# Optimization experiments

Measured on AMD Instinct MI355X. Metric: run time of the kernel, lower is better.

## Reference

```python
import jax, jax.numpy as jnp
import numpy as np

B, T, I, H = 128, 512, 1024, 1024


def _xavier(key, shape):
    # matches torch nn.init.xavier_uniform_
    fan_in, fan_out = shape
    limit = float(np.sqrt(6.0 / (fan_in + fan_out)))
    return jax.random.uniform(key, shape, jnp.float32, -limit, limit)


def setup_inputs() -> dict:
    key = jax.random.key(0)
    ks = jax.random.split(key, 9)
    x = jax.random.normal(ks[0], (B, T, I), dtype=jnp.float32)
    names = ['W_ii', 'W_hi', 'W_if', 'W_hf', 'W_ig', 'W_hg', 'W_io', 'W_ho']
    inp = {'x': x}
    for k, name in zip(ks[1:], names):
        shape = (I, H) if name[2] == 'i' else (H, H)
        inp[name] = _xavier(k, shape)
    for bname in ['b_ii', 'b_hi', 'b_if', 'b_hf', 'b_ig', 'b_hg', 'b_io', 'b_ho']:
        inp[bname] = jnp.zeros((H,), dtype=jnp.float32)
    return inp


def reference(x, W_ii, b_ii, W_hi, b_hi, W_if, b_if, W_hf, b_hf,
              W_ig, b_ig, W_hg, b_hg, W_io, b_io, W_ho, b_ho):
    """LSTM over x [B, T, I]; returns final (h_t, c_t), each [B, H].
    Faithful to the module's per-gate math (input gate i, forget gate f,
    cell candidate g with tanh, output gate o with sigmoid), zero init state.
    Gates are fused into one input GEMM per step group: precompute x @ W_i*
    for all timesteps at once, then scan the recurrence."""
    batch, seq, _ = x.shape
    hidden = W_hi.shape[0]
    # Precompute input projections for all timesteps: [T, B, 4H]
    W_in = jnp.concatenate([W_ii, W_if, W_ig, W_io], axis=1)          # [I, 4H]
    b_in = jnp.concatenate([b_ii + b_hi, b_if + b_hf, b_ig + b_hg, b_io + b_ho])
    x_proj = jnp.einsum('bti,ih->tbh', x, W_in) + b_in                # [T, B, 4H]
    W_h = jnp.concatenate([W_hi, W_hf, W_hg, W_ho], axis=1)           # [H, 4H]

    def step(carry, xp):
        h, c = carry
        gates = xp + h @ W_h                                          # [B, 4H]
        i_t = jax.nn.sigmoid(gates[:, 0 * hidden:1 * hidden])
        f_t = jax.nn.sigmoid(gates[:, 1 * hidden:2 * hidden])
        g_t = jnp.tanh(gates[:, 2 * hidden:3 * hidden])
        o_t = jax.nn.sigmoid(gates[:, 3 * hidden:4 * hidden])
        c = f_t * c + i_t * g_t
        h = o_t * jnp.tanh(c)
        return (h, c), None

    h0 = jnp.zeros((batch, hidden), dtype=x.dtype)
    c0 = jnp.zeros((batch, hidden), dtype=x.dtype)
    (h_t, c_t), _ = jax.lax.scan(step, (h0, c0), x_proj)
    return (h_t, c_t)
```

## Files before the change

### kernel.cpp

```cpp
#include <hip/hip_runtime.h>
#include <cstdint>
#include <cstddef>


#define B_  128
#define T_  512
#define I_  1024
#define H_  1024
#define G4_ 4096
#define SLOTG 32768ull

typedef __attribute__((ext_vector_type(8))) short short8;
typedef __attribute__((ext_vector_type(4))) float f32x4;
typedef unsigned long long u64;

static __device__ __forceinline__ unsigned short f2bf(float f) {
    unsigned u = __builtin_bit_cast(unsigned, f);
    u += 0x7fffu + ((u >> 16) & 1u);
    return (unsigned short)(u >> 16);
}
static __device__ __forceinline__ float bf2f(unsigned short s) {
    unsigned u = (unsigned)s << 16;
    return __builtin_bit_cast(float, u);
}
static __device__ __forceinline__ float sigm(float x) {
    return 1.0f / (1.0f + exp2f(-1.4426950408889634f * x));
}
static __device__ __forceinline__ float tanh_(float x) {
    float e = exp2f(2.8853900817779268f * x);
    return 1.0f - 2.0f / (e + 1.0f);
}
static __device__ __forceinline__ f32x4 mfma16(short8 a, short8 b, f32x4 c) {
    return __builtin_amdgcn_mfma_f32_16x16x32_bf16(a, b, c, 0, 0, 0);
}
static __device__ __forceinline__ bool hasff(u64 v) {
    u64 x = ~v;
    return ((x - 0x0001000100010001ull) & ~x & 0x8000800080008000ull) != 0ull;
}

__global__ __launch_bounds__(256) void pack_w(const float* __restrict__ W,
                                              unsigned short* __restrict__ outBt,
                                              int g) {
    __shared__ float tile[64][65];
    const int tid = threadIdx.x;
    const int k0 = blockIdx.y * 64;
    const int j0 = blockIdx.x * 64;
    {
        const int r  = tid >> 2;
        const int c0 = (tid & 3) * 16;
        const float* src = W + (size_t)(k0 + r) * H_ + j0 + c0;
        #pragma unroll
        for (int q = 0; q < 4; ++q) {
            float4 v = *(const float4*)(src + q * 4);
            tile[r][c0 + q*4 + 0] = v.x;
            tile[r][c0 + q*4 + 1] = v.y;
            tile[r][c0 + q*4 + 2] = v.z;
            tile[r][c0 + q*4 + 3] = v.w;
        }
    }
    __syncthreads();
    {
        const int jl   = tid >> 2;
        const int kseg = (tid & 3) * 16;
        unsigned short* orow = outBt + ((size_t)(j0 + jl) * 4 + g) * 1024 + (k0 + kseg);
        #pragma unroll
        for (int q = 0; q < 16; q += 4) {
            ushort4 u;
            u.x = f2bf(tile[kseg + q + 0][jl]);
            u.y = f2bf(tile[kseg + q + 1][jl]);
            u.z = f2bf(tile[kseg + q + 2][jl]);
            u.w = f2bf(tile[kseg + q + 3][jl]);
            *(ushort4*)(orow + q) = u;
        }
    }
}

__global__ __launch_bounds__(256) void pack_bias(
    const float* b0x, const float* b0h, const float* b1x, const float* b1h,
    const float* b2x, const float* b2h, const float* b3x, const float* b3h,
    float* __restrict__ out) {
    int jc = blockIdx.x * 256 + threadIdx.x;
    int g = jc & 3, jh = jc >> 2;
    const float* bx = (g == 0) ? b0x : (g == 1) ? b1x : (g == 2) ? b2x : b3x;
    const float* bh = (g == 0) ? b0h : (g == 1) ? b1h : (g == 2) ? b2h : b3h;
    out[jc] = bx[jh] + bh[jh];
}

__global__ __launch_bounds__(256) void convert_x(const float* __restrict__ x,
                                                 unsigned short* __restrict__ xb,
                                                 int t0, int Tcc) {
    int e = blockIdx.x * 256 + threadIdx.x;
    int i = (e & 127) << 3;
    int r = e >> 7;
    int b = r / Tcc, tc = r - b * Tcc;
    const float* s = x + (size_t)(b * T_ + t0 + tc) * I_ + i;
    float4 v0 = *(const float4*)s;
    float4 v1 = *(const float4*)(s + 4);
    ushort4 u0; u0.x = f2bf(v0.x); u0.y = f2bf(v0.y); u0.z = f2bf(v0.z); u0.w = f2bf(v0.w);
    ushort4 u1; u1.x = f2bf(v1.x); u1.y = f2bf(v1.y); u1.z = f2bf(v1.z); u1.w = f2bf(v1.w);
    unsigned short* d = xb + (size_t)r * I_ + i;
    *(ushort4*)d = u0;
    *(ushort4*)(d + 4) = u1;
}

__global__ __launch_bounds__(256) void gemm_xproj(
    const unsigned short* __restrict__ A,
    const unsigned short* __restrict__ Bt,
    const float* __restrict__ bias,
    unsigned short* __restrict__ xp,
    int Tcc) {
    const int tid = threadIdx.x;
    const int w = tid >> 6, l = tid & 63;
    const int l15 = l & 15, hi = l >> 4;
    const int row0 = blockIdx.y * 64;
    const int col0 = blockIdx.x * 256 + w * 64;
    const int k0 = hi * 8;
    f32x4 acc[4][4] = {};
    const unsigned short* a0 = A  + (size_t)(row0 + l15) * 1024 + k0;
    const unsigned short* b0 = Bt + (size_t)(col0 + l15) * 1024 + k0;
    for (int ks = 0; ks < 1024; ks += 32) {
        short8 a[4], bb[4];
        #pragma unroll
        for (int mi = 0; mi < 4; ++mi) a[mi]  = *(const short8*)(a0 + (size_t)mi * 16 * 1024 + ks);
        #pragma unroll
        for (int ni = 0; ni < 4; ++ni) bb[ni] = *(const short8*)(b0 + (size_t)ni * 16 * 1024 + ks);
        #pragma unroll
        for (int mi = 0; mi < 4; ++mi)
            #pragma unroll
            for (int ni = 0; ni < 4; ++ni)
                acc[mi][ni] = mfma16(a[mi], bb[ni], acc[mi][ni]);
    }
    #pragma unroll
    for (int mi = 0; mi < 4; ++mi) {
        #pragma unroll
        for (int ni = 0; ni < 4; ++ni) {
            int colg = col0 + ni * 16 + l15;
            float bs = bias[colg];
            #pragma unroll
            for (int j = 0; j < 4; ++j) {
                int r = row0 + mi * 16 + hi * 4 + j;
                int b = r / Tcc, tc = r - b * Tcc;
                xp[(size_t)(tc * 128 + b) * G4_ + colg] = f2bf(acc[mi][ni][j] + bs);
            }
        }
    }
}

__global__ __launch_bounds__(1024, 4) void lstm_recur(
    const unsigned short* __restrict__ Whp,
    const unsigned short* __restrict__ xp,
    u64* __restrict__ hring,
    float* __restrict__ cbuf,
    float* __restrict__ outp,
    int Tcc, int is_last_chunk) {
    __shared__ char hlds[32768];
    __shared__ float gl[16][132];
    __shared__ unsigned short hstage[16][32];

    const int tid = threadIdx.x;
    const int wv = tid >> 6, l = tid & 63;
    const int l15 = l & 15, hi = l >> 4;
    const int ct = wv & 7, kh = wv >> 3;
    const int grp = blockIdx.x >> 5;
    const int cb  = blockIdx.x & 31;
    const int row0 = grp * 16;

    short8 wf[16];
    {
        const unsigned short* wb = Whp + (size_t)(cb * 128 + ct * 16 + l15) * 1024
                                       + kh * 512 + hi * 8;
        #pragma unroll
        for (int ks = 0; ks < 16; ++ks) wf[ks] = *(const short8*)(wb + ks * 32);
    }

    const int erow = tid >> 5, ejh = tid & 31;
    float creg = 0.f;
    if (tid < 512) creg = cbuf[(size_t)(row0 + erow) * H_ + cb * 32 + ejh];

    const int gcol = (tid & 63) * 4;

    for (int st = 0; st < Tcc; ++st) {
        ushort4 xv = {0, 0, 0, 0};
        if (tid < 512)
            xv = *(const ushort4*)(xp + ((size_t)st * 128 + row0 + erow) * G4_
                                      + cb * 128 + ejh * 4);

        u64 g0, g1, g2, g3;
        {
            u64* rp = hring + (size_t)st * SLOTG + (size_t)(row0 + wv) * 256 + gcol;
            for (int it = 0; ; ++it) {
                if (it < 64) {
                    g0 = __hip_atomic_load(rp + 0, __ATOMIC_RELAXED, __HIP_MEMORY_SCOPE_AGENT);
                    g1 = __hip_atomic_load(rp + 1, __ATOMIC_RELAXED, __HIP_MEMORY_SCOPE_AGENT);
                    g2 = __hip_atomic_load(rp + 2, __ATOMIC_RELAXED, __HIP_MEMORY_SCOPE_AGENT);
                    g3 = __hip_atomic_load(rp + 3, __ATOMIC_RELAXED, __HIP_MEMORY_SCOPE_AGENT);
                } else {
                    g0 = __hip_atomic_fetch_add(rp + 0, 0ull, __ATOMIC_RELAXED, __HIP_MEMORY_SCOPE_AGENT);
                    g1 = __hip_atomic_fetch_add(rp + 1, 0ull, __ATOMIC_RELAXED, __HIP_MEMORY_SCOPE_AGENT);
                    g2 = __hip_atomic_fetch_add(rp + 2, 0ull, __ATOMIC_RELAXED, __HIP_MEMORY_SCOPE_AGENT);
                    g3 = __hip_atomic_fetch_add(rp + 3, 0ull, __ATOMIC_RELAXED, __HIP_MEMORY_SCOPE_AGENT);
                }
                if (!(hasff(g0) | hasff(g1) | hasff(g2) | hasff(g3))) break;
                __builtin_amdgcn_s_sleep(1);
            }
        }
        {
            int base = wv * 2048 + gcol * 8;
            int sw = (wv & 7) << 4;
            *(u64*)(hlds + ((base +  0) ^ sw)) = g0;
            *(u64*)(hlds + ((base +  8) ^ sw)) = g1;
            *(u64*)(hlds + ((base + 16) ^ sw)) = g2;
            *(u64*)(hlds + ((base + 24) ^ sw)) = g3;
        }
        __syncthreads();

        f32x4 acc = {};
        {
            const int abase = l15 * 2048 + kh * 1024 + hi * 16;
            const int sw = (l15 & 7) << 4;
            #pragma unroll
            for (int ks = 0; ks < 16; ++ks) {
                short8 a = *(const short8*)(hlds + ((abase + ks * 64) ^ sw));
                acc = mfma16(a, wf[ks], acc);
            }
        }
        if (kh == 0) {
            #pragma unroll
            for (int j = 0; j < 4; ++j) gl[hi * 4 + j][ct * 16 + l15] = acc[j];
        }
        __syncthreads();
        if (kh == 1) {
            #pragma unroll
            for (int j = 0; j < 4; ++j) gl[hi * 4 + j][ct * 16 + l15] += acc[j];
        }
        __syncthreads();

        if (tid < 512) {
            float gi = gl[erow][ejh * 4 + 0] + bf2f(xv.x);
            float gf = gl[erow][ejh * 4 + 1] + bf2f(xv.y);
            float gg = gl[erow][ejh * 4 + 2] + bf2f(xv.z);
            float go = gl[erow][ejh * 4 + 3] + bf2f(xv.w);
            float it = sigm(gi), ft = sigm(gf), gt = tanh_(gg), ot = sigm(go);
            float cn = ft * creg + it * gt;
            float hn = ot * tanh_(cn);
            creg = cn;
            hstage[erow][ejh] = f2bf(hn);
            if (is_last_chunk && st == Tcc - 1) {
                size_t oidx = (size_t)(row0 + erow) * H_ + cb * 32 + ejh;
                outp[oidx] = hn;
                outp[(size_t)B_ * H_ + oidx] = cn;
            }
        }
        __syncthreads();
        if (tid < 128) {
            int prow = tid >> 3, seg = tid & 7;
            u64 hv = *(const u64*)(&hstage[prow][seg * 4]);
            u64* wp = hring + (size_t)(st + 1) * SLOTG
                            + (size_t)(row0 + prow) * 256 + cb * 8 + seg;
            (void)__hip_atomic_exchange(wp, hv, __ATOMIC_RELAXED, __HIP_MEMORY_SCOPE_AGENT);
        }
    }
    if (tid < 512)
        cbuf[(size_t)(row0 + erow) * H_ + cb * 32 + ejh] = creg;
}

extern "C" void kernel_launch(void* const* d_in, const int* in_sizes, int n_in,
                              void* d_out, int out_size, void* d_ws, size_t ws_size,
                              hipStream_t stream) {
    const float* x = (const float*)d_in[0];
    const float* Wx[4] = {(const float*)d_in[1], (const float*)d_in[3],
                          (const float*)d_in[5], (const float*)d_in[7]};
    const float* Wh[4] = {(const float*)d_in[2], (const float*)d_in[4],
                          (const float*)d_in[6], (const float*)d_in[8]};
    const float* bx[4] = {(const float*)d_in[9],  (const float*)d_in[11],
                          (const float*)d_in[13], (const float*)d_in[15]};
    const float* bh[4] = {(const float*)d_in[10], (const float*)d_in[12],
                          (const float*)d_in[14], (const float*)d_in[16]};

    char* p = (char*)d_ws;
    auto take = [&](size_t bytes) {
        char* q = p; p += (bytes + 255) & ~(size_t)255; return q;
    };
    unsigned short* Winp = (unsigned short*)take((size_t)G4_ * 1024 * 2);
    unsigned short* Whp  = (unsigned short*)take((size_t)G4_ * 1024 * 2);
    float*          bias = (float*)take(G4_ * 4);
    float*          cbuf = (float*)take((size_t)B_ * H_ * 4);
    size_t fixed = (size_t)(p - (char*)d_ws);
    size_t per = (size_t)B_ * I_ * 2 + (size_t)B_ * G4_ * 2 + SLOTG * 8 + 768;
    size_t avail = ws_size > fixed + SLOTG * 8 ? ws_size - fixed - SLOTG * 8 : 0;
    int Tc = (int)(avail / per);
    if (Tc > T_) Tc = T_;
    if (Tc < 1) Tc = 1;
    unsigned short* xb    = (unsigned short*)take((size_t)Tc * B_ * I_ * 2);
    unsigned short* xpc   = (unsigned short*)take((size_t)Tc * B_ * G4_ * 2);
    u64*            hring = (u64*)take((size_t)(Tc + 1) * SLOTG * 8);

    for (int g = 0; g < 4; ++g) {
        pack_w<<<dim3(16, 16), 256, 0, stream>>>(Wx[g], Winp, g);
        pack_w<<<dim3(16, 16), 256, 0, stream>>>(Wh[g], Whp, g);
    }
    pack_bias<<<16, 256, 0, stream>>>(bx[0], bh[0], bx[1], bh[1],
                                      bx[2], bh[2], bx[3], bh[3], bias);
    hipMemsetAsync(cbuf, 0, (size_t)B_ * H_ * 4, stream);

    int prev_last = -1;
    for (int t0 = 0; t0 < T_; t0 += Tc) {
        int Tcc = (T_ - t0 < Tc) ? (T_ - t0) : Tc;
        int last = (t0 + Tcc >= T_) ? 1 : 0;
        if (prev_last < 0)
            hipMemsetAsync(hring, 0, SLOTG * 8, stream);
        else
            hipMemcpyAsync(hring, hring + (size_t)prev_last * SLOTG,
                           SLOTG * 8, hipMemcpyDeviceToDevice, stream);
        hipMemsetAsync(hring + SLOTG, 0xFF, (size_t)Tcc * SLOTG * 8, stream);
        convert_x<<<Tcc * 64, 256, 0, stream>>>(x, xb, t0, Tcc);
        gemm_xproj<<<dim3(16, 2 * Tcc), 256, 0, stream>>>(xb, Winp, bias, xpc, Tcc);
        lstm_recur<<<256, 1024, 0, stream>>>(Whp, xpc, hring, cbuf,
                                             (float*)d_out, Tcc, last);
        prev_last = Tcc;
    }
}
```

Before: 3.957 ms.

## Restructure LSTM recurrence block, fuse x conversion into GEMM, drop ring memsets

The recurrent kernel drops to 512 threads per block. Each wave covers 64 gate columns over a quarter of K, so a 4-way partial-sum reduction in LDS replaces the two-pass sum over two K halves. It also polls wider vectors of h with backoff sleeps. The fp32 to bf16 conversion of x moves into the input-projection GEMM, which uses perm truncation instead of round-to-nearest. The GEMM also writes the 0xFF sentinel values into the h ring, so the per-chunk memset and memcpy go away: the final h of each chunk is written into slot 0. The eight weight-pack launches are merged into one. The changes aim to cut launch overhead, extra memory passes and per-step sync latency, at the cost of slightly different bf16 rounding of x and a different occupancy balance in the recurrence.

```diff
diff --git a/kernel.cpp b/kernel.cpp
--- a/kernel.cpp
+++ b/kernel.cpp
@@ -12,6 +12,7 @@
 
 typedef __attribute__((ext_vector_type(8))) short short8;
 typedef __attribute__((ext_vector_type(4))) float f32x4;
+typedef __attribute__((ext_vector_type(2))) unsigned long long u64x2;
 typedef unsigned long long u64;
 
 static __device__ __forceinline__ unsigned short f2bf(float f) {
@@ -33,14 +34,20 @@
 static __device__ __forceinline__ f32x4 mfma16(short8 a, short8 b, f32x4 c) {
     return __builtin_amdgcn_mfma_f32_16x16x32_bf16(a, b, c, 0, 0, 0);
 }
-static __device__ __forceinline__ bool hasff(u64 v) {
-    u64 x = ~v;
-    return ((x - 0x0001000100010001ull) & ~x & 0x8000800080008000ull) != 0ull;
-}
-
-__global__ __launch_bounds__(256) void pack_w(const float* __restrict__ W,
-                                              unsigned short* __restrict__ outBt,
-                                              int g) {
+static __device__ __forceinline__ u64 ffbits(u64 v) {
+    return ((~v) - 0x0001000100010001ull) & v & 0x8000800080008000ull;
+}
+#define AL(p)  __hip_atomic_load((p), __ATOMIC_RELAXED, __HIP_MEMORY_SCOPE_AGENT)
+#define ARMW(p) __hip_atomic_fetch_add((p), 0ull, __ATOMIC_RELAXED, __HIP_MEMORY_SCOPE_AGENT)
+
+__global__ __launch_bounds__(256) void pack_w8(
+    const float* w0, const float* w1, const float* w2, const float* w3,
+    const float* w4, const float* w5, const float* w6, const float* w7,
+    unsigned short* __restrict__ Winp, unsigned short* __restrict__ Whp) {
+    const float* ws[8] = {w0, w1, w2, w3, w4, w5, w6, w7};
+    const float* W = ws[blockIdx.z];
+    unsigned short* dst = (blockIdx.z < 4) ? Winp : Whp;
+    const int g = blockIdx.z & 3;
     __shared__ float tile[64][65];
     const int tid = threadIdx.x;
     const int k0 = blockIdx.y * 64;
@@ -62,7 +69,7 @@
     {
         const int jl   = tid >> 2;
         const int kseg = (tid & 3) * 16;
-        unsigned short* orow = outBt + ((size_t)(j0 + jl) * 4 + g) * 1024 + (k0 + kseg);
+        unsigned short* orow = dst + ((size_t)(j0 + jl) * 4 + g) * 1024 + (k0 + kseg);
         #pragma unroll
         for (int q = 0; q < 16; q += 4) {
             ushort4 u;
@@ -86,42 +93,45 @@
     out[jc] = bx[jh] + bh[jh];
 }
 
-__global__ __launch_bounds__(256) void convert_x(const float* __restrict__ x,
-                                                 unsigned short* __restrict__ xb,
-                                                 int t0, int Tcc) {
-    int e = blockIdx.x * 256 + threadIdx.x;
-    int i = (e & 127) << 3;
-    int r = e >> 7;
-    int b = r / Tcc, tc = r - b * Tcc;
-    const float* s = x + (size_t)(b * T_ + t0 + tc) * I_ + i;
-    float4 v0 = *(const float4*)s;
-    float4 v1 = *(const float4*)(s + 4);
-    ushort4 u0; u0.x = f2bf(v0.x); u0.y = f2bf(v0.y); u0.z = f2bf(v0.z); u0.w = f2bf(v0.w);
-    ushort4 u1; u1.x = f2bf(v1.x); u1.y = f2bf(v1.y); u1.z = f2bf(v1.z); u1.w = f2bf(v1.w);
-    unsigned short* d = xb + (size_t)r * I_ + i;
-    *(ushort4*)d = u0;
-    *(ushort4*)(d + 4) = u1;
-}
-
 __global__ __launch_bounds__(256) void gemm_xproj(
-    const unsigned short* __restrict__ A,
+    const float* __restrict__ x,
     const unsigned short* __restrict__ Bt,
     const float* __restrict__ bias,
     unsigned short* __restrict__ xp,
-    int Tcc) {
+    u64* __restrict__ sent,
+    int t0, int Tcc) {
     const int tid = threadIdx.x;
     const int w = tid >> 6, l = tid & 63;
     const int l15 = l & 15, hi = l >> 4;
     const int row0 = blockIdx.y * 64;
     const int col0 = blockIdx.x * 256 + w * 64;
     const int k0 = hi * 8;
+    const float* xr[4];
+    #pragma unroll
+    for (int mi = 0; mi < 4; ++mi) {
+        int r = row0 + mi * 16 + l15;
+        int b = r / Tcc, tc = r - b * Tcc;
+        xr[mi] = x + ((size_t)b * T_ + t0 + tc) * I_ + k0;
+    }
     f32x4 acc[4][4] = {};
-    const unsigned short* a0 = A  + (size_t)(row0 + l15) * 1024 + k0;
     const unsigned short* b0 = Bt + (size_t)(col0 + l15) * 1024 + k0;
     for (int ks = 0; ks < 1024; ks += 32) {
         short8 a[4], bb[4];
         #pragma unroll
-        for (int mi = 0; mi < 4; ++mi) a[mi]  = *(const short8*)(a0 + (size_t)mi * 16 * 1024 + ks);
+        for (int mi = 0; mi < 4; ++mi) {
+            float4 u = *(const float4*)(xr[mi] + ks);
+            float4 v = *(const float4*)(xr[mi] + ks + 4);
+            unsigned d0 = __builtin_amdgcn_perm(__builtin_bit_cast(unsigned, u.y),
+                                                __builtin_bit_cast(unsigned, u.x), 0x07060302u);
+            unsigned d1 = __builtin_amdgcn_perm(__builtin_bit_cast(unsigned, u.w),
+                                                __builtin_bit_cast(unsigned, u.z), 0x07060302u);
+            unsigned d2 = __builtin_amdgcn_perm(__builtin_bit_cast(unsigned, v.y),
+                                                __builtin_bit_cast(unsigned, v.x), 0x07060302u);
+            unsigned d3 = __builtin_amdgcn_perm(__builtin_bit_cast(unsigned, v.w),
+                                                __builtin_bit_cast(unsigned, v.z), 0x07060302u);
+            uint4 pk = {d0, d1, d2, d3};
+            a[mi] = __builtin_bit_cast(short8, pk);
+        }
         #pragma unroll
         for (int ni = 0; ni < 4; ++ni) bb[ni] = *(const short8*)(b0 + (size_t)ni * 16 * 1024 + ks);
         #pragma unroll
@@ -144,124 +154,146 @@
             }
         }
     }
-}
-
-__global__ __launch_bounds__(1024, 4) void lstm_recur(
+    {
+        size_t sidx = ((size_t)(blockIdx.y * gridDim.x + blockIdx.x) * 256 + tid) * 4;
+        u64* sp = sent + sidx;
+        sp[0] = ~0ull; sp[1] = ~0ull; sp[2] = ~0ull; sp[3] = ~0ull;
+    }
+}
+
+__global__ __launch_bounds__(512, 2) void lstm_recur(
     const unsigned short* __restrict__ Whp,
     const unsigned short* __restrict__ xp,
     u64* __restrict__ hring,
     float* __restrict__ cbuf,
     float* __restrict__ outp,
-    int Tcc, int is_last_chunk) {
-    __shared__ char hlds[32768];
-    __shared__ float gl[16][132];
-    __shared__ unsigned short hstage[16][32];
-
-    const int tid = threadIdx.x;
-    const int wv = tid >> 6, l = tid & 63;
+    int Tcc, int is_last) {
+    __shared__ __align__(16) char hlds[32768];
+    __shared__ __align__(16) float gl[4][16][140];
+
+    const int t = threadIdx.x;
+    const int w = t >> 6, l = t & 63;
     const int l15 = l & 15, hi = l >> 4;
-    const int ct = wv & 7, kh = wv >> 3;
-    const int grp = blockIdx.x >> 5;
-    const int cb  = blockIdx.x & 31;
+    const int cw = w & 1, kq = w >> 1;
+    const int grp = blockIdx.x >> 5, cb = blockIdx.x & 31;
     const int row0 = grp * 16;
 
-    short8 wf[16];
+    short8 wf[4][8];
     {
-        const unsigned short* wb = Whp + (size_t)(cb * 128 + ct * 16 + l15) * 1024
-                                       + kh * 512 + hi * 8;
-        #pragma unroll
-        for (int ks = 0; ks < 16; ++ks) wf[ks] = *(const short8*)(wb + ks * 32);
-    }
-
-    const int erow = tid >> 5, ejh = tid & 31;
-    float creg = 0.f;
-    if (tid < 512) creg = cbuf[(size_t)(row0 + erow) * H_ + cb * 32 + ejh];
-
-    const int gcol = (tid & 63) * 4;
+        const unsigned short* wb = Whp + (size_t)(cb * 128 + cw * 64 + l15) * 1024
+                                       + kq * 256 + hi * 8;
+        #pragma unroll
+        for (int ci = 0; ci < 4; ++ci)
+            #pragma unroll
+            for (int ks = 0; ks < 8; ++ks)
+                wf[ci][ks] = *(const short8*)(wb + ci * 16 * 1024 + ks * 32);
+    }
+
+    const int urow = t & 15, uq = t >> 4;
+    float4 creg = {0.f, 0.f, 0.f, 0.f};
+    if (t < 128)
+        creg = *(const float4*)&cbuf[(size_t)(row0 + urow) * H_ + cb * 32 + uq * 4];
+
+    const int prow = t & 15, pko = t >> 4;
 
     for (int st = 0; st < Tcc; ++st) {
-        ushort4 xv = {0, 0, 0, 0};
-        if (tid < 512)
-            xv = *(const ushort4*)(xp + ((size_t)st * 128 + row0 + erow) * G4_
-                                      + cb * 128 + ejh * 4);
-
-        u64 g0, g1, g2, g3;
+        unsigned short xv[16];
+        if (t < 128) {
+            const unsigned short* xq = xp + ((size_t)st * 128 + row0 + urow) * G4_
+                                          + cb * 128 + uq * 16;
+            *(uint4*)&xv[0] = *(const uint4*)xq;
+            *(uint4*)&xv[8] = *(const uint4*)(xq + 8);
+        }
+
+        u64 q[8];
         {
-            u64* rp = hring + (size_t)st * SLOTG + (size_t)(row0 + wv) * 256 + gcol;
-            for (int it = 0; ; ++it) {
+            u64* rp = hring + (size_t)st * SLOTG + (size_t)(row0 + prow) * 256 + pko * 2;
+            int it = 0;
+            for (;;) {
                 if (it < 64) {
-                    g0 = __hip_atomic_load(rp + 0, __ATOMIC_RELAXED, __HIP_MEMORY_SCOPE_AGENT);
-                    g1 = __hip_atomic_load(rp + 1, __ATOMIC_RELAXED, __HIP_MEMORY_SCOPE_AGENT);
-                    g2 = __hip_atomic_load(rp + 2, __ATOMIC_RELAXED, __HIP_MEMORY_SCOPE_AGENT);
-                    g3 = __hip_atomic_load(rp + 3, __ATOMIC_RELAXED, __HIP_MEMORY_SCOPE_AGENT);
+                    q[0] = AL(rp);       q[1] = AL(rp + 1);
+                    q[2] = AL(rp + 64);  q[3] = AL(rp + 65);
+                    q[4] = AL(rp + 128); q[5] = AL(rp + 129);
+                    q[6] = AL(rp + 192); q[7] = AL(rp + 193);
                 } else {
-                    g0 = __hip_atomic_fetch_add(rp + 0, 0ull, __ATOMIC_RELAXED, __HIP_MEMORY_SCOPE_AGENT);
-                    g1 = __hip_atomic_fetch_add(rp + 1, 0ull, __ATOMIC_RELAXED, __HIP_MEMORY_SCOPE_AGENT);
-                    g2 = __hip_atomic_fetch_add(rp + 2, 0ull, __ATOMIC_RELAXED, __HIP_MEMORY_SCOPE_AGENT);
-                    g3 = __hip_atomic_fetch_add(rp + 3, 0ull, __ATOMIC_RELAXED, __HIP_MEMORY_SCOPE_AGENT);
+                    q[0] = ARMW(rp);       q[1] = ARMW(rp + 1);
+                    q[2] = ARMW(rp + 64);  q[3] = ARMW(rp + 65);
+                    q[4] = ARMW(rp + 128); q[5] = ARMW(rp + 129);
+                    q[6] = ARMW(rp + 192); q[7] = ARMW(rp + 193);
                 }
-                if (!(hasff(g0) | hasff(g1) | hasff(g2) | hasff(g3))) break;
-                __builtin_amdgcn_s_sleep(1);
-            }
-        }
-        {
-            int base = wv * 2048 + gcol * 8;
-            int sw = (wv & 7) << 4;
-            *(u64*)(hlds + ((base +  0) ^ sw)) = g0;
-            *(u64*)(hlds + ((base +  8) ^ sw)) = g1;
-            *(u64*)(hlds + ((base + 16) ^ sw)) = g2;
-            *(u64*)(hlds + ((base + 24) ^ sw)) = g3;
+                u64 bad = ffbits(q[0]) | ffbits(q[1]) | ffbits(q[2]) | ffbits(q[3])
+                        | ffbits(q[4]) | ffbits(q[5]) | ffbits(q[6]) | ffbits(q[7]);
+                if (!bad) break;
+                ++it;
+                if (it < 16) __builtin_amdgcn_s_sleep(1);
+                else         __builtin_amdgcn_s_sleep(4);
+            }
+        }
+        #pragma unroll
+        for (int j = 0; j < 4; ++j) {
+            u64x2 v = {q[2 * j], q[2 * j + 1]};
+            *(u64x2*)(hlds + (pko + 32 * j) * 256 + prow * 16) = v;
         }
         __syncthreads();
 
-        f32x4 acc = {};
-        {
-            const int abase = l15 * 2048 + kh * 1024 + hi * 16;
-            const int sw = (l15 & 7) << 4;
-            #pragma unroll
-            for (int ks = 0; ks < 16; ++ks) {
-                short8 a = *(const short8*)(hlds + ((abase + ks * 64) ^ sw));
-                acc = mfma16(a, wf[ks], acc);
-            }
-        }
-        if (kh == 0) {
-            #pragma unroll
-            for (int j = 0; j < 4; ++j) gl[hi * 4 + j][ct * 16 + l15] = acc[j];
-        }
+        f32x4 acc[4] = {};
+        #pragma unroll
+        for (int ks = 0; ks < 8; ++ks) {
+            int ko = (kq * 8 + ks) * 4 + hi;
+            short8 a = *(const short8*)(hlds + ko * 256 + l15 * 16);
+            #pragma unroll
+            for (int ci = 0; ci < 4; ++ci)
+                acc[ci] = mfma16(a, wf[ci][ks], acc[ci]);
+        }
+        #pragma unroll
+        for (int ci = 0; ci < 4; ++ci)
+            #pragma unroll
+            for (int j = 0; j < 4; ++j)
+                gl[kq][hi * 4 + j][cw * 64 + ci * 16 + l15] = acc[ci][j];
         __syncthreads();
-        if (kh == 1) {
-            #pragma unroll
-            for (int j = 0; j < 4; ++j) gl[hi * 4 + j][ct * 16 + l15] += acc[j];
-        }
-        __syncthreads();
-
-        if (tid < 512) {
-            float gi = gl[erow][ejh * 4 + 0] + bf2f(xv.x);
-            float gf = gl[erow][ejh * 4 + 1] + bf2f(xv.y);
-            float gg = gl[erow][ejh * 4 + 2] + bf2f(xv.z);
-            float go = gl[erow][ejh * 4 + 3] + bf2f(xv.w);
-            float it = sigm(gi), ft = sigm(gf), gt = tanh_(gg), ot = sigm(go);
-            float cn = ft * creg + it * gt;
-            float hn = ot * tanh_(cn);
-            creg = cn;
-            hstage[erow][ejh] = f2bf(hn);
-            if (is_last_chunk && st == Tcc - 1) {
-                size_t oidx = (size_t)(row0 + erow) * H_ + cb * 32 + ejh;
-                outp[oidx] = hn;
-                outp[(size_t)B_ * H_ + oidx] = cn;
-            }
-        }
-        __syncthreads();
-        if (tid < 128) {
-            int prow = tid >> 3, seg = tid & 7;
-            u64 hv = *(const u64*)(&hstage[prow][seg * 4]);
-            u64* wp = hring + (size_t)(st + 1) * SLOTG
-                            + (size_t)(row0 + prow) * 256 + cb * 8 + seg;
-            (void)__hip_atomic_exchange(wp, hv, __ATOMIC_RELAXED, __HIP_MEMORY_SCOPE_AGENT);
-        }
-    }
-    if (tid < 512)
-        cbuf[(size_t)(row0 + erow) * H_ + cb * 32 + ejh] = creg;
+
+        if (t < 128) {
+            float g16[16];
+            #pragma unroll
+            for (int qq = 0; qq < 4; ++qq) {
+                float4 s = *(const float4*)&gl[0][urow][uq * 16 + qq * 4];
+                #pragma unroll
+                for (int k2 = 1; k2 < 4; ++k2) {
+                    float4 s2 = *(const float4*)&gl[k2][urow][uq * 16 + qq * 4];
+                    s.x += s2.x; s.y += s2.y; s.z += s2.z; s.w += s2.w;
+                }
+                g16[qq * 4 + 0] = s.x; g16[qq * 4 + 1] = s.y;
+                g16[qq * 4 + 2] = s.z; g16[qq * 4 + 3] = s.w;
+            }
+            unsigned short hb[4];
+            float cn4[4], hn4[4];
+            #pragma unroll
+            for (int qq = 0; qq < 4; ++qq) {
+                float gi = g16[qq * 4 + 0] + bf2f(xv[qq * 4 + 0]);
+                float gf = g16[qq * 4 + 1] + bf2f(xv[qq * 4 + 1]);
+                float gg = g16[qq * 4 + 2] + bf2f(xv[qq * 4 + 2]);
+                float go = g16[qq * 4 + 3] + bf2f(xv[qq * 4 + 3]);
+                float it_ = sigm(gi), ft = sigm(gf), gt = tanh_(gg), ot = sigm(go);
+                float co = (qq == 0) ? creg.x : (qq == 1) ? creg.y : (qq == 2) ? creg.z : creg.w;
+                float cn = ft * co + it_ * gt;
+                float hn = ot * tanh_(cn);
+                cn4[qq] = cn; hn4[qq] = hn; hb[qq] = f2bf(hn);
+            }
+            creg.x = cn4[0]; creg.y = cn4[1]; creg.z = cn4[2]; creg.w = cn4[3];
+            u64 hw = (u64)hb[0] | ((u64)hb[1] << 16) | ((u64)hb[2] << 32) | ((u64)hb[3] << 48);
+            int dst = (st == Tcc - 1) ? 0 : st + 1;
+            u64* wp = hring + (size_t)dst * SLOTG + (size_t)(row0 + urow) * 256
+                            + cb * 8 + uq;
+            (void)__hip_atomic_exchange(wp, hw, __ATOMIC_RELAXED, __HIP_MEMORY_SCOPE_AGENT);
+            if (is_last && st == Tcc - 1) {
+                size_t o = (size_t)(row0 + urow) * H_ + cb * 32 + uq * 4;
+                *(float4*)&outp[o] = {hn4[0], hn4[1], hn4[2], hn4[3]};
+                *(float4*)&outp[(size_t)B_ * H_ + o] = creg;
+            }
+        }
+    }
+    if (t < 128)
+        *(float4*)&cbuf[(size_t)(row0 + urow) * H_ + cb * 32 + uq * 4] = creg;
 }
 
 extern "C" void kernel_launch(void* const* d_in, const int* in_sizes, int n_in,
@@ -285,38 +317,28 @@
     unsigned short* Whp  = (unsigned short*)take((size_t)G4_ * 1024 * 2);
     float*          bias = (float*)take(G4_ * 4);
     float*          cbuf = (float*)take((size_t)B_ * H_ * 4);
-    size_t fixed = (size_t)(p - (char*)d_ws);
-    size_t per = (size_t)B_ * I_ * 2 + (size_t)B_ * G4_ * 2 + SLOTG * 8 + 768;
-    size_t avail = ws_size > fixed + SLOTG * 8 ? ws_size - fixed - SLOTG * 8 : 0;
+    size_t fixed = (size_t)(p - (char*)d_ws) + SLOTG * 8 + 512;
+    size_t per = (size_t)B_ * G4_ * 2 + SLOTG * 8 + 512;
+    size_t avail = ws_size > fixed ? ws_size - fixed : 0;
     int Tc = (int)(avail / per);
     if (Tc > T_) Tc = T_;
     if (Tc < 1) Tc = 1;
-    unsigned short* xb    = (unsigned short*)take((size_t)Tc * B_ * I_ * 2);
     unsigned short* xpc   = (unsigned short*)take((size_t)Tc * B_ * G4_ * 2);
     u64*            hring = (u64*)take((size_t)(Tc + 1) * SLOTG * 8);
 
-    for (int g = 0; g < 4; ++g) {
-        pack_w<<<dim3(16, 16), 256, 0, stream>>>(Wx[g], Winp, g);
-        pack_w<<<dim3(16, 16), 256, 0, stream>>>(Wh[g], Whp, g);
-    }
+    pack_w8<<<dim3(16, 16, 8), 256, 0, stream>>>(
+        Wx[0], Wx[1], Wx[2], Wx[3], Wh[0], Wh[1], Wh[2], Wh[3], Winp, Whp);
     pack_bias<<<16, 256, 0, stream>>>(bx[0], bh[0], bx[1], bh[1],
                                       bx[2], bh[2], bx[3], bh[3], bias);
-    hipMemsetAsync(cbuf, 0, (size_t)B_ * H_ * 4, stream);
-
-    int prev_last = -1;
+    (void)hipMemsetAsync(hring, 0, SLOTG * 8, stream);
+    (void)hipMemsetAsync(cbuf, 0, (size_t)B_ * H_ * 4, stream);
+
     for (int t0 = 0; t0 < T_; t0 += Tc) {
         int Tcc = (T_ - t0 < Tc) ? (T_ - t0) : Tc;
         int last = (t0 + Tcc >= T_) ? 1 : 0;
-        if (prev_last < 0)
-            hipMemsetAsync(hring, 0, SLOTG * 8, stream);
-        else
-            hipMemcpyAsync(hring, hring + (size_t)prev_last * SLOTG,
-                           SLOTG * 8, hipMemcpyDeviceToDevice, stream);
-        hipMemsetAsync(hring + SLOTG, 0xFF, (size_t)Tcc * SLOTG * 8, stream);
-        convert_x<<<Tcc * 64, 256, 0, stream>>>(x, xb, t0, Tcc);
-        gemm_xproj<<<dim3(16, 2 * Tcc), 256, 0, stream>>>(xb, Winp, bias, xpc, Tcc);
-        lstm_recur<<<256, 1024, 0, stream>>>(Whp, xpc, hring, cbuf,
-                                             (float*)d_out, Tcc, last);
-        prev_last = Tcc;
-    }
-}
+        gemm_xproj<<<dim3(16, 2 * Tcc), 256, 0, stream>>>(
+            x, Winp, bias, xpc, hring + SLOTG, t0, Tcc);
+        lstm_recur<<<256, 512, 0, stream>>>(Whp, xpc, hring, cbuf,
+                                            (float*)d_out, Tcc, last);
+    }
+}
```

Measured after the change: 7.024 ms. +77.5%, slower.
